# Performance work log

Hardware: AMD Instinct MI355X
Metric: run time of the kernel (lower is better)

## Reference

```python
import jax, jax.numpy as jnp
import numpy as np

T = 24
ML = 10.0   # storage capacity constant `ml` from the repo
A_PEN = 10.0  # penalty weight `A`


def setup_inputs() -> dict:
    key = jax.random.key(0)
    k1, k2 = jax.random.split(key)
    B = 1 << 20
    out = jax.random.normal(k1, (B, T), dtype=jnp.float32)
    var_y = jax.random.normal(k2, (B, 2 * T), dtype=jnp.float32)
    return {"out": out, "var_y": var_y}


def _hinge(z):
    # (sign(z)+1)/2 * |z|  ==  max(z, 0) with torch's sign/abs grad semantics
    return (jnp.sign(z) + 1.0) * 0.5 * jnp.abs(z)


def reference(out, var_y):
    p = var_y[:, :T]          # prices  [B, T]
    a = var_y[:, T:]          # demand  [B, T]
    delta = out               # control [B, T]

    # recurrent state x0 after step t is cumsum(delta); at step t the loop
    # uses the *previous* x0 (0 at t=0)
    cum = jnp.cumsum(delta, axis=1)
    x0_prev = jnp.concatenate(
        [jnp.zeros_like(delta[:, :1]), cum[:, :-1]], axis=1)  # [B, T]

    # min_value_0 term only exists for t >= 1
    t_mask = (jnp.arange(T) >= 1).astype(delta.dtype)  # [T]

    min_v0 = _hinge(-delta - a) * t_mask
    max_v1 = _hinge(-delta - x0_prev)
    min_v1 = _hinge(x0_prev + delta - ML)

    pen = (min_v0 + max_v1 + min_v1) * A_PEN
    bill = jnp.abs(a + delta) * p + pen        # [B, T]
    # loop does cost += mean_over_batch(bill_t) for each t
    cost = jnp.sum(jnp.mean(bill, axis=0))
    return cost
```

## Files before the change

kernel.cpp:

```cpp
#include <hip/hip_runtime.h>


constexpr int TT = 24;
constexpr float ML_C = 10.0f;
constexpr float A_PEN_C = 10.0f;

constexpr int LPR = 4;
constexpr int EPL = 6;
constexpr int RPW = 64 / LPR;
constexpr int NBLK = 1024;
constexpr int NTHR = 256;

__global__ __launch_bounds__(NTHR)
void pen_partial_kernel(const float* __restrict__ dout,
                        const float* __restrict__ vary,
                        float* __restrict__ partial,
                        int B, float invB) {
    const int tid  = threadIdx.x;
    const int lane = tid & 63;
    const int sub  = lane & (LPR - 1);
    const int g    = lane >> 2;

    const int nWaves   = gridDim.x * (NTHR / 64);
    const int waveId   = blockIdx.x * (NTHR / 64) + (tid >> 6);
    const int RG       = (B + RPW - 1) / RPW;

    float s = 0.0f;

    for (int it = waveId; it < RG; it += nWaves) {
        const int rg  = RG - 1 - it;
        const long long row = (long long)rg * RPW + g;
        if (row >= B) continue;

        const float* dp = dout + row * TT + EPL * sub;
        const float* vp = vary + row * (2 * TT) + EPL * sub;
        const float* ap = vp + TT;
        float2 d01 = *(const float2*)(dp);
        float2 d23 = *(const float2*)(dp + 2);
        float2 d45 = *(const float2*)(dp + 4);
        float2 p01 = *(const float2*)(vp);
        float2 p23 = *(const float2*)(vp + 2);
        float2 p45 = *(const float2*)(vp + 4);
        float2 a01 = *(const float2*)(ap);
        float2 a23 = *(const float2*)(ap + 2);
        float2 a45 = *(const float2*)(ap + 4);

        float d[EPL] = {d01.x, d01.y, d23.x, d23.y, d45.x, d45.y};
        float p[EPL] = {p01.x, p01.y, p23.x, p23.y, p45.x, p45.y};
        float a[EPL] = {a01.x, a01.y, a23.x, a23.y, a45.x, a45.y};

        const float localsum = ((d[0] + d[1]) + (d[2] + d[3])) + (d[4] + d[5]);
        float incl = localsum;
        float t1 = __shfl_up(incl, 1, LPR);
        if (sub >= 1) incl += t1;
        float t2 = __shfl_up(incl, 2, LPR);
        if (sub >= 2) incl += t2;
        float x0 = incl - localsum;

        #pragma unroll
        for (int j = 0; j < EPL; ++j) {
            const float dd = d[j];
            const float aa = a[j];
            float mv0 = fmaxf(-dd - aa, 0.0f);
            if (j == 0 && sub == 0) mv0 = 0.0f;
            const float mx1 = fmaxf(-dd - x0, 0.0f);
            const float mv1 = fmaxf(x0 + dd - ML_C, 0.0f);
            s += fabsf(aa + dd) * p[j] + (mv0 + mx1 + mv1) * A_PEN_C;
            x0 += dd;
        }
    }

    #pragma unroll
    for (int off = 32; off > 0; off >>= 1)
        s += __shfl_down(s, off, 64);
    __shared__ float ws[NTHR / 64];
    if (lane == 0) ws[tid >> 6] = s;
    __syncthreads();
    if (tid == 0) {
        float b = 0.0f;
        #pragma unroll
        for (int w = 0; w < NTHR / 64; ++w) b += ws[w];
        partial[blockIdx.x] = b * invB;
    }
}

__global__ __launch_bounds__(256)
void pen_final_reduce_kernel(const float* __restrict__ partial,
                             float* __restrict__ out, int n) {
    const int tid = threadIdx.x;
    float s = 0.0f;
    for (int i = tid; i < n; i += 256) s += partial[i];
    #pragma unroll
    for (int off = 32; off > 0; off >>= 1)
        s += __shfl_down(s, off, 64);
    __shared__ float ws[4];
    if ((tid & 63) == 0) ws[tid >> 6] = s;
    __syncthreads();
    if (tid == 0) out[0] = ws[0] + ws[1] + ws[2] + ws[3];
}

extern "C" void kernel_launch(void* const* d_in, const int* in_sizes, int n_in,
                              void* d_out, int out_size, void* d_ws, size_t ws_size,
                              hipStream_t stream) {
    const float* dout = (const float*)d_in[0];
    const float* vary = (const float*)d_in[1];
    const int B = in_sizes[0] / TT;
    float* partial = (float*)d_ws;

    pen_partial_kernel<<<NBLK, NTHR, 0, stream>>>(dout, vary, partial, B, 1.0f / (float)B);
    pen_final_reduce_kernel<<<1, 256, 0, stream>>>(partial, (float*)d_out, NBLK);
}
```

Baseline: 338.7 us.

## Use two lanes per row with float4 loads and a single-shuffle prefix scan

Each row is now split across 2 lanes of 12 elements instead of 4 lanes of 6. Loads become 16-byte float4 instead of 8-byte float2, and the prefix-sum exchange drops to one shuffle. The block count is doubled to keep enough waves in flight. Per-lane register use rises and the per-lane access stride grows, which may reduce coalescing efficiency.

```diff
diff --git a/kernel.cpp b/kernel.cpp
--- a/kernel.cpp
+++ b/kernel.cpp
@@ -5,10 +5,10 @@
 constexpr float ML_C = 10.0f;
 constexpr float A_PEN_C = 10.0f;
 
-constexpr int LPR = 4;
-constexpr int EPL = 6;
+constexpr int LPR = 2;
+constexpr int EPL = 12;
 constexpr int RPW = 64 / LPR;
-constexpr int NBLK = 1024;
+constexpr int NBLK = 2048;
 constexpr int NTHR = 256;
 
 __global__ __launch_bounds__(NTHR)
@@ -19,7 +19,7 @@
     const int tid  = threadIdx.x;
     const int lane = tid & 63;
     const int sub  = lane & (LPR - 1);
-    const int g    = lane >> 2;
+    const int g    = lane >> 1;
 
     const int nWaves   = gridDim.x * (NTHR / 64);
     const int waveId   = blockIdx.x * (NTHR / 64) + (tid >> 6);
@@ -35,27 +35,24 @@
         const float* dp = dout + row * TT + EPL * sub;
         const float* vp = vary + row * (2 * TT) + EPL * sub;
         const float* ap = vp + TT;
-        float2 d01 = *(const float2*)(dp);
-        float2 d23 = *(const float2*)(dp + 2);
-        float2 d45 = *(const float2*)(dp + 4);
-        float2 p01 = *(const float2*)(vp);
-        float2 p23 = *(const float2*)(vp + 2);
-        float2 p45 = *(const float2*)(vp + 4);
-        float2 a01 = *(const float2*)(ap);
-        float2 a23 = *(const float2*)(ap + 2);
-        float2 a45 = *(const float2*)(ap + 4);
+        float4 d0 = *(const float4*)(dp);
+        float4 d1 = *(const float4*)(dp + 4);
+        float4 d2 = *(const float4*)(dp + 8);
+        float4 p0 = *(const float4*)(vp);
+        float4 p1 = *(const float4*)(vp + 4);
+        float4 p2 = *(const float4*)(vp + 8);
+        float4 a0 = *(const float4*)(ap);
+        float4 a1 = *(const float4*)(ap + 4);
+        float4 a2 = *(const float4*)(ap + 8);
 
-        float d[EPL] = {d01.x, d01.y, d23.x, d23.y, d45.x, d45.y};
-        float p[EPL] = {p01.x, p01.y, p23.x, p23.y, p45.x, p45.y};
-        float a[EPL] = {a01.x, a01.y, a23.x, a23.y, a45.x, a45.y};
+        float d[EPL] = {d0.x, d0.y, d0.z, d0.w, d1.x, d1.y, d1.z, d1.w, d2.x, d2.y, d2.z, d2.w};
+        float p[EPL] = {p0.x, p0.y, p0.z, p0.w, p1.x, p1.y, p1.z, p1.w, p2.x, p2.y, p2.z, p2.w};
+        float a[EPL] = {a0.x, a0.y, a0.z, a0.w, a1.x, a1.y, a1.z, a1.w, a2.x, a2.y, a2.z, a2.w};
 
-        const float localsum = ((d[0] + d[1]) + (d[2] + d[3])) + (d[4] + d[5]);
-        float incl = localsum;
-        float t1 = __shfl_up(incl, 1, LPR);
-        if (sub >= 1) incl += t1;
-        float t2 = __shfl_up(incl, 2, LPR);
-        if (sub >= 2) incl += t2;
-        float x0 = incl - localsum;
+        const float localsum = (((d[0] + d[1]) + (d[2] + d[3])) + ((d[4] + d[5]) + (d[6] + d[7])))
+                             + ((d[8] + d[9]) + (d[10] + d[11]));
+        const float prev = __shfl_up(localsum, 1, LPR);
+        float x0 = (sub == 1) ? prev : 0.0f;
 
         #pragma unroll
         for (int j = 0; j < EPL; ++j) {
```

Result: no change. 341.2 us (+0.7%).
